# Kernel optimization log

Measured on AMD Instinct MI355X. Metric: run time of the kernel, lower is better.

## Reference

```python
import jax, jax.numpy as jnp
import numpy as np

EPS = 1e-6

def elu_feature_map(x):
    return jax.nn.elu(x) + 1.0

def setup_inputs() -> dict:
    key = jax.random.key(0)
    kq, kk, kv = jax.random.split(key, 3)
    B, N, L, S, H, D, M = 4, 8, 1024, 1024, 8, 64, 64
    queries = jax.random.normal(kq, (B, N, L, H, D), dtype=jnp.float32)
    keys = jax.random.normal(kk, (B, N, S, H, D), dtype=jnp.float32)
    values = jax.random.normal(kv, (B, N, S, H, M), dtype=jnp.float32)
    key_mask = jnp.ones((B, S), dtype=jnp.float32)  # key_lengths.float_matrix (all valid)
    return {"queries": queries, "keys": keys, "values": values, "key_mask": key_mask}

def reference(queries, keys, values, key_mask):
    # Q: [B,N,L,H,D], K: [B,N,S,H,D], V: [B,N,S,H,M], key_mask: [B,S]
    Q = elu_feature_map(queries)
    K = elu_feature_map(keys) * key_mask[:, None, :, None, None]
    # KV state: [B,N,H,M,D]
    KV = jnp.einsum('bnshd,bnshm->bnhmd', K, values)
    # normalizer: [B,N,L,H]
    Z = 1.0 / (jnp.einsum('bnlhd,bnhd->bnlh', Q, K.sum(axis=2)) + EPS)
    # output: [B,N,L,H,M]
    V = jnp.einsum('bnlhd,bnhmd,bnlh->bnlhm', Q, KV, Z)
    return V
```

## Files before the change

kernel.cpp:

```cpp
#include <hip/hip_runtime.h>
#include <hip/hip_bf16.h>


constexpr int Bc = 4, Nc = 8, Hc = 8;
constexpr int Lc = 1024, Sc = 1024, Dc = 64, Mc = 64;
constexpr int HD = Hc * Dc;
constexpr int GROUPS = Bc * Nc * Hc;
constexpr int LSPLITS = 4;
constexpr int LROWS = Lc / LSPLITS;
constexpr int PARTIAL = Dc * Mc + Dc;
constexpr int NTL = LROWS / 64;
constexpr int PADS = 36;
constexpr int PADD = 68;
constexpr float EPSF = 1e-6f;

typedef __attribute__((ext_vector_type(8))) __bf16 bf16x8;
typedef __attribute__((ext_vector_type(4))) float f32x4;

__device__ __forceinline__ float elup1(float x) {
    return x > 0.0f ? x + 1.0f : __expf(x);
}
__device__ __forceinline__ unsigned short f2bf(float f) {
    unsigned u = __builtin_bit_cast(unsigned, f);
    u += 0x7fffu + ((u >> 16) & 1u);
    return (unsigned short)(u >> 16);
}
__device__ __forceinline__ float bf2f(unsigned short h) {
    return __builtin_bit_cast(float, (unsigned)h << 16);
}
__device__ __forceinline__ void splitbf(float x, unsigned short& h, unsigned short& l) {
    h = f2bf(x);
    l = f2bf(x - bf2f(h));
}
__device__ __forceinline__ unsigned pack2(unsigned short lo, unsigned short hi) {
    return (unsigned)lo | ((unsigned)hi << 16);
}
__device__ __forceinline__ bf16x8 ones_frag() {
    union { bf16x8 v; unsigned short s[8]; } u;
    #pragma unroll
    for (int i = 0; i < 8; ++i) u.s[i] = 0x3F80;
    return u.v;
}

template<int NSPL>
__global__ void __launch_bounds__(256, 4)
la_kv_mfma(const float* __restrict__ Kg, const float* __restrict__ Vg,
           const float* __restrict__ Mg, float* __restrict__ ws)
{
    constexpr int SR = Sc / NSPL;
    constexpr int NT = SR / 32;

    __shared__ unsigned short kth[2][Dc][PADS];
    __shared__ unsigned short ktl[2][Dc][PADS];
    __shared__ unsigned short vth[2][Dc][PADS];
    __shared__ unsigned short vtl[2][Dc][PADS];

    const int t    = threadIdx.x;
    const int tx   = t & 15;
    const int tyq  = t >> 4;
    const int lane = t & 63;
    const int w    = t >> 6;
    const int g    = blockIdx.y;
    const int sp   = blockIdx.x;
    const int h    = g & 7;
    const int bn   = g >> 3;
    const int b    = g >> 6;

    const size_t rowbase = (size_t)bn * Sc * HD + (size_t)h * Dc;
    const size_t mbase   = (size_t)b * Sc;
    const int    sbase   = sp * SR;

    float4 kA0, kA1, vA0, vA1; float2 mA;
    float4 kB0, kB1, vB0, vB1; float2 mB;

    auto loadA_A = [&](int it) {
        const int s0 = sbase + it * 32 + 2 * tyq;
        const size_t off = rowbase + (size_t)s0 * HD + 4 * tx;
        kA0 = *reinterpret_cast<const float4*>(Kg + off);
        kA1 = *reinterpret_cast<const float4*>(Kg + off + HD);
        vA0 = *reinterpret_cast<const float4*>(Vg + off);
        vA1 = *reinterpret_cast<const float4*>(Vg + off + HD);
        mA  = *reinterpret_cast<const float2*>(Mg + mbase + s0);
    };
    auto loadA_B = [&](int it) {
        const int s0 = sbase + it * 32 + 2 * tyq;
        const size_t off = rowbase + (size_t)s0 * HD + 4 * tx;
        kB0 = *reinterpret_cast<const float4*>(Kg + off);
        kB1 = *reinterpret_cast<const float4*>(Kg + off + HD);
        vB0 = *reinterpret_cast<const float4*>(Vg + off);
        vB1 = *reinterpret_cast<const float4*>(Vg + off + HD);
        mB  = *reinterpret_cast<const float2*>(Mg + mbase + s0);
    };
    auto stage = [&](int buf, const float4& K0, const float4& K1,
                     const float4& V0, const float4& V1, const float2& M2) {
        const float k0[4] = {K0.x, K0.y, K0.z, K0.w};
        const float k1[4] = {K1.x, K1.y, K1.z, K1.w};
        const float v0[4] = {V0.x, V0.y, V0.z, V0.w};
        const float v1[4] = {V1.x, V1.y, V1.z, V1.w};
        #pragma unroll
        for (int i = 0; i < 4; ++i) {
            const float a0 = elup1(k0[i]) * M2.x;
            const float a1 = elup1(k1[i]) * M2.y;
            unsigned short h0, l0, h1, l1;
            splitbf(a0, h0, l0);
            splitbf(a1, h1, l1);
            *reinterpret_cast<unsigned*>(&kth[buf][4 * tx + i][2 * tyq]) = pack2(h0, h1);
            *reinterpret_cast<unsigned*>(&ktl[buf][4 * tx + i][2 * tyq]) = pack2(l0, l1);
            unsigned short vh0, vl0, vh1, vl1;
            splitbf(v0[i], vh0, vl0);
            splitbf(v1[i], vh1, vl1);
            *reinterpret_cast<unsigned*>(&vth[buf][4 * tx + i][2 * tyq]) = pack2(vh0, vh1);
            *reinterpret_cast<unsigned*>(&vtl[buf][4 * tx + i][2 * tyq]) = pack2(vl0, vl1);
        }
    };

    f32x4 acc[4], aks;
    #pragma unroll
    for (int ms = 0; ms < 4; ++ms) acc[ms] = (f32x4){0.f, 0.f, 0.f, 0.f};
    aks = (f32x4){0.f, 0.f, 0.f, 0.f};
    const bf16x8 ones = ones_frag();

    const int fcol = 8 * (lane >> 4);
    const int frow = lane & 15;

    auto compute = [&](int buf) {
        union { bf16x8 v; uint2 u[2]; } fah, fal;
        {
            const uint2* ph = reinterpret_cast<const uint2*>(&kth[buf][16 * w + frow][fcol]);
            fah.u[0] = ph[0]; fah.u[1] = ph[1];
            const uint2* pl = reinterpret_cast<const uint2*>(&ktl[buf][16 * w + frow][fcol]);
            fal.u[0] = pl[0]; fal.u[1] = pl[1];
        }
        aks = __builtin_amdgcn_mfma_f32_16x16x32_bf16(fah.v, ones, aks, 0, 0, 0);
        aks = __builtin_amdgcn_mfma_f32_16x16x32_bf16(fal.v, ones, aks, 0, 0, 0);
        #pragma unroll
        for (int ms = 0; ms < 4; ++ms) {
            union { bf16x8 v; uint2 u[2]; } fbh, fbl;
            const uint2* ph = reinterpret_cast<const uint2*>(&vth[buf][16 * ms + frow][fcol]);
            fbh.u[0] = ph[0]; fbh.u[1] = ph[1];
            const uint2* pl = reinterpret_cast<const uint2*>(&vtl[buf][16 * ms + frow][fcol]);
            fbl.u[0] = pl[0]; fbl.u[1] = pl[1];
            acc[ms] = __builtin_amdgcn_mfma_f32_16x16x32_bf16(fah.v, fbh.v, acc[ms], 0, 0, 0);
            acc[ms] = __builtin_amdgcn_mfma_f32_16x16x32_bf16(fah.v, fbl.v, acc[ms], 0, 0, 0);
            acc[ms] = __builtin_amdgcn_mfma_f32_16x16x32_bf16(fal.v, fbh.v, acc[ms], 0, 0, 0);
        }
    };

    loadA_A(0);
    loadA_B(1);
    stage(0, kA0, kA1, vA0, vA1, mA);
    loadA_A(2);
    __syncthreads();

    for (int it = 0; it < NT; it += 2) {
        compute(0);
        stage(1, kB0, kB1, vB0, vB1, mB);
        if (it + 3 < NT) loadA_B(it + 3);
        __syncthreads();

        compute(1);
        if (it + 2 < NT) stage(0, kA0, kA1, vA0, vA1, mA);
        if (it + 4 < NT) loadA_A(it + 4);
        __syncthreads();
    }

    float* outp = ws + (size_t)(g * NSPL + sp) * PARTIAL;
    #pragma unroll
    for (int ms = 0; ms < 4; ++ms)
        #pragma unroll
        for (int r = 0; r < 4; ++r)
            outp[(16 * w + 4 * (lane >> 4) + r) * Mc + 16 * ms + frow] = acc[ms][r];

    if (frow == 0) {
        #pragma unroll
        for (int r = 0; r < 4; ++r)
            outp[Dc * Mc + 16 * w + 4 * (lane >> 4) + r] = aks[r];
    }
}

template<int NSPL>
__global__ void __launch_bounds__(256, 4)
la_out_mfma(const float* __restrict__ Qg, const float* __restrict__ ws,
            float* __restrict__ Og)
{
    __shared__ unsigned short kvh[Mc][PADD];
    __shared__ unsigned short kvl[Mc][PADD];
    __shared__ unsigned short ksh[64];
    __shared__ unsigned short ksl[64];
    __shared__ unsigned short qhh[64][PADD];
    __shared__ unsigned short qll[64][PADD];

    const int t    = threadIdx.x;
    const int tx   = t & 15;
    const int tyq  = t >> 4;
    const int lane = t & 63;
    const int w    = t >> 6;
    const int g    = blockIdx.y;
    const int ls   = blockIdx.x;
    const int h    = g & 7;
    const int bn   = g >> 3;

    const size_t rowbase = (size_t)bn * Lc * HD + (size_t)h * Dc;
    const float* pw = ws + (size_t)g * NSPL * PARTIAL;
    const int lbase = ls * LROWS;

    float4 qr[4];
    auto loadB = [&](int it) {
        const int l0 = lbase + it * 64 + 4 * tyq;
        #pragma unroll
        for (int j = 0; j < 4; ++j)
            qr[j] = *reinterpret_cast<const float4*>(Qg + rowbase + (size_t)(l0 + j) * HD + 4 * tx);
    };
    auto storeB = [&]() {
        #pragma unroll
        for (int j = 0; j < 4; ++j) {
            const int r = 4 * tyq + j;
            const float q[4] = {qr[j].x, qr[j].y, qr[j].z, qr[j].w};
            unsigned short h0, l0, h1, l1, h2, l2, h3, l3;
            splitbf(elup1(q[0]), h0, l0);
            splitbf(elup1(q[1]), h1, l1);
            splitbf(elup1(q[2]), h2, l2);
            splitbf(elup1(q[3]), h3, l3);
            uint2 ph, pl;
            ph.x = pack2(h0, h1); ph.y = pack2(h2, h3);
            pl.x = pack2(l0, l1); pl.y = pack2(l2, l3);
            *reinterpret_cast<uint2*>(&qhh[r][4 * tx]) = ph;
            *reinterpret_cast<uint2*>(&qll[r][4 * tx]) = pl;
        }
    };

    loadB(0);
    #pragma unroll
    for (int e = 0; e < 16; ++e) {
        const int idx = t + 256 * e;
        float s = 0.f;
        #pragma unroll
        for (int sp = 0; sp < NSPL; ++sp) s += pw[sp * PARTIAL + idx];
        unsigned short hh, ll;
        splitbf(s, hh, ll);
        kvh[idx & 63][idx >> 6] = hh;
        kvl[idx & 63][idx >> 6] = ll;
    }
    if (t < 64) {
        float s = 0.f;
        #pragma unroll
        for (int sp = 0; sp < NSPL; ++sp) s += pw[sp * PARTIAL + Dc * Mc + t];
        unsigned short hh, ll;
        splitbf(s, hh, ll);
        ksh[t] = hh;
        ksl[t] = ll;
    }
    storeB();
    __syncthreads();

    const int fcol = 8 * (lane >> 4);
    const int frow = lane & 15;
    const size_t obase = (size_t)bn * Lc * HD + (size_t)h * Mc;

    for (int it = 0; it < NTL; ++it) {
        if (it + 1 < NTL) loadB(it + 1);
        union { bf16x8 v; uint2 u[2]; } fah0, fal0, fah1, fal1;
        {
            const uint2* p;
            p = reinterpret_cast<const uint2*>(&qhh[16 * w + frow][fcol]);      fah0.u[0] = p[0]; fah0.u[1] = p[1];
            p = reinterpret_cast<const uint2*>(&qll[16 * w + frow][fcol]);      fal0.u[0] = p[0]; fal0.u[1] = p[1];
            p = reinterpret_cast<const uint2*>(&qhh[16 * w + frow][32 + fcol]); fah1.u[0] = p[0]; fah1.u[1] = p[1];
            p = reinterpret_cast<const uint2*>(&qll[16 * w + frow][32 + fcol]); fal1.u[0] = p[0]; fal1.u[1] = p[1];
        }
        f32x4 acc[4], accz;
        #pragma unroll
        for (int ms = 0; ms < 4; ++ms) acc[ms] = (f32x4){0.f, 0.f, 0.f, 0.f};
        accz = (f32x4){0.f, 0.f, 0.f, 0.f};

        #pragma unroll
        for (int ks = 0; ks < 2; ++ks) {
            const bf16x8 fh = ks ? fah1.v : fah0.v;
            const bf16x8 fl = ks ? fal1.v : fal0.v;
            #pragma unroll
            for (int ms = 0; ms < 4; ++ms) {
                union { bf16x8 v; uint2 u[2]; } fbh, fbl;
                const uint2* ph = reinterpret_cast<const uint2*>(&kvh[16 * ms + frow][32 * ks + fcol]);
                fbh.u[0] = ph[0]; fbh.u[1] = ph[1];
                const uint2* pl = reinterpret_cast<const uint2*>(&kvl[16 * ms + frow][32 * ks + fcol]);
                fbl.u[0] = pl[0]; fbl.u[1] = pl[1];
                acc[ms] = __builtin_amdgcn_mfma_f32_16x16x32_bf16(fh, fbh.v, acc[ms], 0, 0, 0);
                acc[ms] = __builtin_amdgcn_mfma_f32_16x16x32_bf16(fh, fbl.v, acc[ms], 0, 0, 0);
                acc[ms] = __builtin_amdgcn_mfma_f32_16x16x32_bf16(fl, fbh.v, acc[ms], 0, 0, 0);
            }
            union { bf16x8 v; uint2 u[2]; } fzh, fzl;
            const uint2* ph = reinterpret_cast<const uint2*>(&ksh[32 * ks + fcol]);
            fzh.u[0] = ph[0]; fzh.u[1] = ph[1];
            const uint2* pl = reinterpret_cast<const uint2*>(&ksl[32 * ks + fcol]);
            fzl.u[0] = pl[0]; fzl.u[1] = pl[1];
            accz = __builtin_amdgcn_mfma_f32_16x16x32_bf16(fh, fzh.v, accz, 0, 0, 0);
            accz = __builtin_amdgcn_mfma_f32_16x16x32_bf16(fh, fzl.v, accz, 0, 0, 0);
            accz = __builtin_amdgcn_mfma_f32_16x16x32_bf16(fl, fzh.v, accz, 0, 0, 0);
        }

        const int lt = lbase + it * 64 + 16 * w + 4 * (lane >> 4);
        #pragma unroll
        for (int r = 0; r < 4; ++r) {
            const float z = 1.0f / (accz[r] + EPSF);
            const size_t ro = obase + (size_t)(lt + r) * HD + frow;
            #pragma unroll
            for (int ms = 0; ms < 4; ++ms)
                Og[ro + 16 * ms] = acc[ms][r] * z;
        }
        __syncthreads();
        if (it + 1 < NTL) storeB();
        __syncthreads();
    }
}

__global__ void __launch_bounds__(256, 1)
la_fused_kernel(const float* __restrict__ Qg, const float* __restrict__ Kg,
                const float* __restrict__ Vg, const float* __restrict__ Mg,
                float* __restrict__ Og)
{
    __shared__ float lk[32][Dc];
    __shared__ float lv[32][Mc];
    __shared__ float kvt[Dc][Mc];
    __shared__ float ksm[Dc];
    __shared__ float qt[Dc][64];

    const int t  = threadIdx.x;
    const int tx = t & 15;
    const int ty = t >> 4;
    const int g  = blockIdx.x;
    const int h  = g & 7;
    const int bn = g >> 3;
    const int b  = g >> 6;

    const size_t rowbase = (size_t)bn * Sc * HD + (size_t)h * Dc;
    const size_t mbase   = (size_t)b * Sc;

    const int d0 = tx * 4, m0 = ty * 4, c4 = tx * 4, r0 = ty;

    float acc[4][4] = {{0.f,0.f,0.f,0.f},{0.f,0.f,0.f,0.f},{0.f,0.f,0.f,0.f},{0.f,0.f,0.f,0.f}};
    float ks[4] = {0.f, 0.f, 0.f, 0.f};
    float4 kr[2], vr[2];
    float  mr[2];

    auto loadA = [&](int it) {
        const int s0 = it * 32;
        #pragma unroll
        for (int k = 0; k < 2; ++k) {
            const int r = r0 + 16 * k;
            const size_t off = rowbase + (size_t)(s0 + r) * HD + c4;
            kr[k] = *reinterpret_cast<const float4*>(Kg + off);
            vr[k] = *reinterpret_cast<const float4*>(Vg + off);
            mr[k] = Mg[mbase + s0 + r];
        }
    };
    auto storeA = [&]() {
        #pragma unroll
        for (int k = 0; k < 2; ++k) {
            const int r = r0 + 16 * k;
            float4 kk;
            kk.x = elup1(kr[k].x) * mr[k];
            kk.y = elup1(kr[k].y) * mr[k];
            kk.z = elup1(kr[k].z) * mr[k];
            kk.w = elup1(kr[k].w) * mr[k];
            *reinterpret_cast<float4*>(&lk[r][c4]) = kk;
            *reinterpret_cast<float4*>(&lv[r][c4]) = vr[k];
        }
    };

    loadA(0);
    storeA();
    __syncthreads();
    for (int it = 0; it < Sc / 32; ++it) {
        if (it + 1 < Sc / 32) loadA(it + 1);
        #pragma unroll 8
        for (int r = 0; r < 32; ++r) {
            const float4 k4 = *reinterpret_cast<const float4*>(&lk[r][d0]);
            const float4 v4 = *reinterpret_cast<const float4*>(&lv[r][m0]);
            const float kk[4] = {k4.x, k4.y, k4.z, k4.w};
            const float vv[4] = {v4.x, v4.y, v4.z, v4.w};
            ks[0] += kk[0]; ks[1] += kk[1]; ks[2] += kk[2]; ks[3] += kk[3];
            #pragma unroll
            for (int i = 0; i < 4; ++i)
                #pragma unroll
                for (int j = 0; j < 4; ++j)
                    acc[i][j] += kk[i] * vv[j];
        }
        __syncthreads();
        if (it + 1 < Sc / 32) storeA();
        __syncthreads();
    }

    #pragma unroll
    for (int i = 0; i < 4; ++i) {
        float4 w;
        w.x = acc[i][0]; w.y = acc[i][1]; w.z = acc[i][2]; w.w = acc[i][3];
        *reinterpret_cast<float4*>(&kvt[d0 + i][m0]) = w;
    }
    if (ty == 0) {
        #pragma unroll
        for (int i = 0; i < 4; ++i) ksm[d0 + i] = ks[i];
    }
    __syncthreads();

    float4 qr[4];
    auto loadB = [&](int it) {
        const int l0 = it * 64;
        #pragma unroll
        for (int k = 0; k < 4; ++k) {
            const int r = r0 + 16 * k;
            const size_t off = rowbase + (size_t)(l0 + r) * HD + c4;
            qr[k] = *reinterpret_cast<const float4*>(Qg + off);
        }
    };
    const int swzw = (tx & 7) << 2;
    auto storeB = [&]() {
        #pragma unroll
        for (int k = 0; k < 4; ++k) {
            const int r = r0 + 16 * k;
            const int lidx = r ^ swzw;
            qt[c4 + 0][lidx] = elup1(qr[k].x);
            qt[c4 + 1][lidx] = elup1(qr[k].y);
            qt[c4 + 2][lidx] = elup1(qr[k].z);
            qt[c4 + 3][lidx] = elup1(qr[k].w);
        }
    };

    loadB(0);
    storeB();
    __syncthreads();
    for (int it = 0; it < Lc / 64; ++it) {
        if (it + 1 < Lc / 64) loadB(it + 1);
        float accB[4][4] = {{0.f,0.f,0.f,0.f},{0.f,0.f,0.f,0.f},{0.f,0.f,0.f,0.f},{0.f,0.f,0.f,0.f}};
        float za[4] = {0.f, 0.f, 0.f, 0.f};
        #pragma unroll 8
        for (int d = 0; d < Dc; ++d) {
            const int swz = ((d >> 2) & 7) << 2;
            const float4 q4  = *reinterpret_cast<const float4*>(&qt[d][(4 * ty) ^ swz]);
            const float4 kv4 = *reinterpret_cast<const float4*>(&kvt[d][4 * tx]);
            const float kd = ksm[d];
            const float qq[4] = {q4.x, q4.y, q4.z, q4.w};
            const float kv[4] = {kv4.x, kv4.y, kv4.z, kv4.w};
            #pragma unroll
            for (int i = 0; i < 4; ++i) {
                za[i] += qq[i] * kd;
                #pragma unroll
                for (int j = 0; j < 4; ++j)
                    accB[i][j] += qq[i] * kv[j];
            }
        }
        const int l0 = it * 64;
        const size_t obase = (size_t)bn * Lc * HD + (size_t)h * Mc;
        #pragma unroll
        for (int i = 0; i < 4; ++i) {
            const int l = l0 + 4 * ty + i;
            const float z = 1.0f / (za[i] + EPSF);
            float4 o;
            o.x = accB[i][0] * z; o.y = accB[i][1] * z;
            o.z = accB[i][2] * z; o.w = accB[i][3] * z;
            *reinterpret_cast<float4*>(Og + obase + (size_t)l * HD + 4 * tx) = o;
        }
        __syncthreads();
        if (it + 1 < Lc / 64) storeB();
        __syncthreads();
    }
}

extern "C" void kernel_launch(void* const* d_in, const int* in_sizes, int n_in,
                              void* d_out, int out_size, void* d_ws, size_t ws_size,
                              hipStream_t stream) {
    const float* Qg = (const float*)d_in[0];
    const float* Kg = (const float*)d_in[1];
    const float* Vg = (const float*)d_in[2];
    const float* Mg = (const float*)d_in[3];
    float* Og = (float*)d_out;

    const size_t need4 = (size_t)GROUPS * 4 * PARTIAL * sizeof(float);
    if (ws_size >= need4) {
        float* ws = (float*)d_ws;
        hipLaunchKernelGGL((la_kv_mfma<4>), dim3(4, GROUPS), dim3(256), 0, stream,
                           Kg, Vg, Mg, ws);
        hipLaunchKernelGGL((la_out_mfma<4>), dim3(LSPLITS, GROUPS), dim3(256), 0, stream,
                           Qg, ws, Og);
    } else {
        hipLaunchKernelGGL(la_fused_kernel, dim3(GROUPS), dim3(256), 0, stream,
                           Qg, Kg, Vg, Mg, Og);
    }
}
```

Measured before the change: 74.64 us.

## Load K/V fragments directly from global into MFMA registers, dropping LDS staging

The KV-state kernel no longer transposes K and V through double-buffered shared memory. Each lane now reads its MFMA fragment elements straight from global memory, as strided scalar loads, and does the bf16 hi/lo split in registers. This removes LDS traffic and block barriers. In exchange, global loads become uncoalesced scalar reads (stride HD), V is read redundantly by each of the four waves, and the loop (unroll 1) no longer prefetches ahead.

```diff
diff --git a/kernel.cpp b/kernel.cpp
--- a/kernel.cpp
+++ b/kernel.cpp
@@ -10,7 +10,6 @@
 constexpr int LROWS = Lc / LSPLITS;
 constexpr int PARTIAL = Dc * Mc + Dc;
 constexpr int NTL = LROWS / 64;
-constexpr int PADS = 36;
 constexpr int PADD = 68;
 constexpr float EPSF = 1e-6f;
 
@@ -44,22 +43,17 @@
 
 template<int NSPL>
 __global__ void __launch_bounds__(256, 4)
-la_kv_mfma(const float* __restrict__ Kg, const float* __restrict__ Vg,
-           const float* __restrict__ Mg, float* __restrict__ ws)
+la_kv_direct(const float* __restrict__ Kg, const float* __restrict__ Vg,
+             const float* __restrict__ Mg, float* __restrict__ ws)
 {
     constexpr int SR = Sc / NSPL;
     constexpr int NT = SR / 32;
 
-    __shared__ unsigned short kth[2][Dc][PADS];
-    __shared__ unsigned short ktl[2][Dc][PADS];
-    __shared__ unsigned short vth[2][Dc][PADS];
-    __shared__ unsigned short vtl[2][Dc][PADS];
-
     const int t    = threadIdx.x;
-    const int tx   = t & 15;
-    const int tyq  = t >> 4;
     const int lane = t & 63;
     const int w    = t >> 6;
+    const int frow = lane & 15;
+    const int kg   = lane >> 4;
     const int g    = blockIdx.y;
     const int sp   = blockIdx.x;
     const int h    = g & 7;
@@ -70,98 +64,51 @@
     const size_t mbase   = (size_t)b * Sc;
     const int    sbase   = sp * SR;
 
-    float4 kA0, kA1, vA0, vA1; float2 mA;
-    float4 kB0, kB1, vB0, vB1; float2 mB;
-
-    auto loadA_A = [&](int it) {
-        const int s0 = sbase + it * 32 + 2 * tyq;
-        const size_t off = rowbase + (size_t)s0 * HD + 4 * tx;
-        kA0 = *reinterpret_cast<const float4*>(Kg + off);
-        kA1 = *reinterpret_cast<const float4*>(Kg + off + HD);
-        vA0 = *reinterpret_cast<const float4*>(Vg + off);
-        vA1 = *reinterpret_cast<const float4*>(Vg + off + HD);
-        mA  = *reinterpret_cast<const float2*>(Mg + mbase + s0);
-    };
-    auto loadA_B = [&](int it) {
-        const int s0 = sbase + it * 32 + 2 * tyq;
-        const size_t off = rowbase + (size_t)s0 * HD + 4 * tx;
-        kB0 = *reinterpret_cast<const float4*>(Kg + off);
-        kB1 = *reinterpret_cast<const float4*>(Kg + off + HD);
-        vB0 = *reinterpret_cast<const float4*>(Vg + off);
-        vB1 = *reinterpret_cast<const float4*>(Vg + off + HD);
-        mB  = *reinterpret_cast<const float2*>(Mg + mbase + s0);
-    };
-    auto stage = [&](int buf, const float4& K0, const float4& K1,
-                     const float4& V0, const float4& V1, const float2& M2) {
-        const float k0[4] = {K0.x, K0.y, K0.z, K0.w};
-        const float k1[4] = {K1.x, K1.y, K1.z, K1.w};
-        const float v0[4] = {V0.x, V0.y, V0.z, V0.w};
-        const float v1[4] = {V1.x, V1.y, V1.z, V1.w};
-        #pragma unroll
-        for (int i = 0; i < 4; ++i) {
-            const float a0 = elup1(k0[i]) * M2.x;
-            const float a1 = elup1(k1[i]) * M2.y;
-            unsigned short h0, l0, h1, l1;
-            splitbf(a0, h0, l0);
-            splitbf(a1, h1, l1);
-            *reinterpret_cast<unsigned*>(&kth[buf][4 * tx + i][2 * tyq]) = pack2(h0, h1);
-            *reinterpret_cast<unsigned*>(&ktl[buf][4 * tx + i][2 * tyq]) = pack2(l0, l1);
-            unsigned short vh0, vl0, vh1, vl1;
-            splitbf(v0[i], vh0, vl0);
-            splitbf(v1[i], vh1, vl1);
-            *reinterpret_cast<unsigned*>(&vth[buf][4 * tx + i][2 * tyq]) = pack2(vh0, vh1);
-            *reinterpret_cast<unsigned*>(&vtl[buf][4 * tx + i][2 * tyq]) = pack2(vl0, vl1);
-        }
-    };
-
     f32x4 acc[4], aks;
     #pragma unroll
     for (int ms = 0; ms < 4; ++ms) acc[ms] = (f32x4){0.f, 0.f, 0.f, 0.f};
     aks = (f32x4){0.f, 0.f, 0.f, 0.f};
     const bf16x8 ones = ones_frag();
 
-    const int fcol = 8 * (lane >> 4);
-    const int frow = lane & 15;
-
-    auto compute = [&](int buf) {
-        union { bf16x8 v; uint2 u[2]; } fah, fal;
-        {
-            const uint2* ph = reinterpret_cast<const uint2*>(&kth[buf][16 * w + frow][fcol]);
-            fah.u[0] = ph[0]; fah.u[1] = ph[1];
-            const uint2* pl = reinterpret_cast<const uint2*>(&ktl[buf][16 * w + frow][fcol]);
-            fal.u[0] = pl[0]; fal.u[1] = pl[1];
-        }
-        aks = __builtin_amdgcn_mfma_f32_16x16x32_bf16(fah.v, ones, aks, 0, 0, 0);
-        aks = __builtin_amdgcn_mfma_f32_16x16x32_bf16(fal.v, ones, aks, 0, 0, 0);
+    union uf { bf16x8 v; unsigned short s[8]; };
+
+    #pragma unroll 1
+    for (int it = 0; it < NT; ++it) {
+        const int sb = sbase + it * 32 + 8 * kg;
+        const float* kp = Kg + rowbase + (size_t)sb * HD + 16 * w + frow;
+        const float* vp = Vg + rowbase + (size_t)sb * HD + frow;
+        const float* mp = Mg + mbase + sb;
+
+        float ka[8], mk[8], vb[4][8];
+        #pragma unroll
+        for (int j = 0; j < 8; ++j) {
+            ka[j] = kp[j * HD];
+            mk[j] = mp[j];
+        }
+        #pragma unroll
+        for (int ms = 0; ms < 4; ++ms)
+            #pragma unroll
+            for (int j = 0; j < 8; ++j)
+                vb[ms][j] = vp[j * HD + 16 * ms];
+
+        uf kh, kl;
+        #pragma unroll
+        for (int j = 0; j < 8; ++j) {
+            const float a = elup1(ka[j]) * mk[j];
+            splitbf(a, kh.s[j], kl.s[j]);
+        }
+        aks = __builtin_amdgcn_mfma_f32_16x16x32_bf16(kh.v, ones, aks, 0, 0, 0);
+        aks = __builtin_amdgcn_mfma_f32_16x16x32_bf16(kl.v, ones, aks, 0, 0, 0);
         #pragma unroll
         for (int ms = 0; ms < 4; ++ms) {
-            union { bf16x8 v; uint2 u[2]; } fbh, fbl;
-            const uint2* ph = reinterpret_cast<const uint2*>(&vth[buf][16 * ms + frow][fcol]);
-            fbh.u[0] = ph[0]; fbh.u[1] = ph[1];
-            const uint2* pl = reinterpret_cast<const uint2*>(&vtl[buf][16 * ms + frow][fcol]);
-            fbl.u[0] = pl[0]; fbl.u[1] = pl[1];
-            acc[ms] = __builtin_amdgcn_mfma_f32_16x16x32_bf16(fah.v, fbh.v, acc[ms], 0, 0, 0);
-            acc[ms] = __builtin_amdgcn_mfma_f32_16x16x32_bf16(fah.v, fbl.v, acc[ms], 0, 0, 0);
-            acc[ms] = __builtin_amdgcn_mfma_f32_16x16x32_bf16(fal.v, fbh.v, acc[ms], 0, 0, 0);
-        }
-    };
-
-    loadA_A(0);
-    loadA_B(1);
-    stage(0, kA0, kA1, vA0, vA1, mA);
-    loadA_A(2);
-    __syncthreads();
-
-    for (int it = 0; it < NT; it += 2) {
-        compute(0);
-        stage(1, kB0, kB1, vB0, vB1, mB);
-        if (it + 3 < NT) loadA_B(it + 3);
-        __syncthreads();
-
-        compute(1);
-        if (it + 2 < NT) stage(0, kA0, kA1, vA0, vA1, mA);
-        if (it + 4 < NT) loadA_A(it + 4);
-        __syncthreads();
+            uf vh, vl;
+            #pragma unroll
+            for (int j = 0; j < 8; ++j)
+                splitbf(vb[ms][j], vh.s[j], vl.s[j]);
+            acc[ms] = __builtin_amdgcn_mfma_f32_16x16x32_bf16(kh.v, vh.v, acc[ms], 0, 0, 0);
+            acc[ms] = __builtin_amdgcn_mfma_f32_16x16x32_bf16(kh.v, vl.v, acc[ms], 0, 0, 0);
+            acc[ms] = __builtin_amdgcn_mfma_f32_16x16x32_bf16(kl.v, vh.v, acc[ms], 0, 0, 0);
+        }
     }
 
     float* outp = ws + (size_t)(g * NSPL + sp) * PARTIAL;
@@ -476,7 +423,7 @@
     const size_t need4 = (size_t)GROUPS * 4 * PARTIAL * sizeof(float);
     if (ws_size >= need4) {
         float* ws = (float*)d_ws;
-        hipLaunchKernelGGL((la_kv_mfma<4>), dim3(4, GROUPS), dim3(256), 0, stream,
+        hipLaunchKernelGGL((la_kv_direct<4>), dim3(4, GROUPS), dim3(256), 0, stream,
                            Kg, Vg, Mg, ws);
         hipLaunchKernelGGL((la_out_mfma<4>), dim3(LSPLITS, GROUPS), dim3(256), 0, stream,
                            Qg, ws, Og);
```

Result: slower. 80.89 us (+8.4%).
